# Optimization experiments

Hardware: AMD Instinct MI355X
Metric: run time of the kernel (lower is better)

## Reference

```python
import jax, jax.numpy as jnp
import numpy as np

D = 1024
N_HEAD = 16
D_HEAD = D // N_HEAD
EPS = 1e-6


def setup_inputs() -> dict:
    key = jax.random.key(0)
    k1, k2, k3 = jax.random.split(key, 3)
    x = jax.random.normal(k1, (4, 1024, D), dtype=jnp.float32)
    # Linear weights stored as (in, out); y = x @ W
    Wqkv = jax.random.normal(k2, (D, 3 * D), dtype=jnp.float32) * (1.0 / np.sqrt(D))
    Wo = jax.random.normal(k3, (D, D), dtype=jnp.float32) * (1.0 / np.sqrt(D))
    scale_q = jnp.ones((D_HEAD,), dtype=jnp.float32)
    scale_k = jnp.ones((D_HEAD,), dtype=jnp.float32)
    return {"x": x, "Wqkv": Wqkv, "Wo": Wo, "scale_q": scale_q, "scale_k": scale_k}


def _rmsnorm_global(x, scale):
    # NOTE: faithful to source: mean over ALL elements (scalar RMS), not per-vector.
    rms = jnp.sqrt(jnp.mean(x * x))
    return (x / (rms + EPS)) * scale  # scale broadcasts over last dim (d_head)


def reference(x, Wqkv, Wo, scale_q, scale_k):
    b, s, d = x.shape
    qkv = x @ Wqkv  # (b, s, 3d)
    q, k, v = jnp.split(qkv, 3, axis=-1)
    q = q.reshape(b, s, N_HEAD, D_HEAD)
    k = k.reshape(b, s, N_HEAD, D_HEAD)
    v = v.reshape(b, s, N_HEAD, D_HEAD)
    q = _rmsnorm_global(q, scale_q)
    k = _rmsnorm_global(k, scale_k)
    # NOTE: no 1/sqrt(d_head) scaling, no mask (faithful to source)
    attn = jnp.einsum('bqhd,bkhd->bhqk', q, k)
    attn = jax.nn.softmax(attn, axis=-1)
    z = jnp.einsum('bhqk,bkhd->bqhd', attn, v)
    z = z.reshape(b, s, d)
    return z @ Wo
```

## Files before the change

### kernel.cpp

```cpp
#include <hip/hip_runtime.h>

typedef float f32x4 __attribute__((ext_vector_type(4)));
typedef short bf16x8 __attribute__((ext_vector_type(8)));
typedef _Float16 f16x8 __attribute__((ext_vector_type(8)));
typedef unsigned short u16;

__device__ __forceinline__ u16 f2bf(float f) {
  unsigned int u = __float_as_uint(f);
  u = u + 0x7fffu + ((u >> 16) & 1u);
  return (u16)(u >> 16);
}
__device__ __forceinline__ float bf2f(u16 h) {
  return __uint_as_float(((unsigned int)h) << 16);
}
__device__ __forceinline__ u16 f2h(float f) {
  _Float16 h = (_Float16)f;
  union { _Float16 h; u16 u; } cv;
  cv.h = h;
  return cv.u;
}

typedef unsigned int as1_uint __attribute__((address_space(1)));
typedef unsigned int as3_uint __attribute__((address_space(3)));
__device__ __forceinline__ void gl_lds16(const void* g, void* l) {
  __builtin_amdgcn_global_load_lds((as1_uint*)g, (as3_uint*)l, 16, 0, 0);
}


__global__ __launch_bounds__(256) void conv_x_kernel(const float* __restrict__ x,
                                                     u16* __restrict__ Xp) {
  const int g = blockIdx.x * 256 + threadIdx.x;
  const int o = g * 8;
  const int slab = o >> 17;
  const int rem = o & 131071;
  const int kstep = rem >> 12;
  const int rem2 = rem & 4095;
  const int r = rem2 >> 5;
  const int cp = (rem2 & 31) >> 3;
  const int c = cp ^ ((r >> 1) & 3);
  const int s = slab * 128 + r;
  const int k = kstep * 32 + c * 8;
  const float4 v0 = *(const float4*)&x[(size_t)s * 1024 + k];
  const float4 v1 = *(const float4*)&x[(size_t)s * 1024 + k + 4];
  ushort4 a, b;
  a.x = f2h(v0.x); a.y = f2h(v0.y); a.z = f2h(v0.z); a.w = f2h(v0.w);
  b.x = f2h(v1.x); b.y = f2h(v1.y); b.z = f2h(v1.z); b.w = f2h(v1.w);
  *(ushort4*)&Xp[o] = a;
  *(ushort4*)&Xp[o + 4] = b;
}

__global__ __launch_bounds__(256) void conv_w_kernel(
    const float* __restrict__ src, int ncols, u16* __restrict__ dst) {
  __shared__ float tl[64][132];
  const int t = threadIdx.x;
  const int slab = blockIdx.x, kg = blockIdx.y;
  const int n0 = slab * 128, k0 = kg * 64;
#pragma unroll
  for (int i = 0; i < 8; i++) {
    const int fidx = i * 256 + t;
    const int r = fidx >> 5, c4 = (fidx & 31) * 4;
    *(float4*)&tl[r][c4] = *(const float4*)&src[(size_t)(k0 + r) * ncols + n0 + c4];
  }
  __syncthreads();
  const size_t base = (size_t)slab * 131072 + (size_t)(kg * 2) * 4096;
#pragma unroll
  for (int i = 0; i < 4; i++) {
    const int g = i * 256 + t;
    const int img = g >> 9, ci = g & 511;
    const int r = ci >> 2, cp = ci & 3;
    const int c = cp ^ ((r >> 1) & 3);
    const int klc = img * 32 + c * 8;
    ushort4 h0, h1;
    float v[8];
#pragma unroll
    for (int e = 0; e < 8; e++) v[e] = tl[klc + e][r];
    h0.x = f2h(v[0]); h0.y = f2h(v[1]); h0.z = f2h(v[2]); h0.w = f2h(v[3]);
    h1.x = f2h(v[4]); h1.y = f2h(v[5]); h1.z = f2h(v[6]); h1.w = f2h(v[7]);
    *(ushort4*)&dst[base + g * 8] = h0;
    *(ushort4*)&dst[base + g * 8 + 4] = h1;
  }
}

__global__ __launch_bounds__(512, 2) void gemm_qkv_kernel(
    const u16* __restrict__ Xp, const u16* __restrict__ Wp,
    u16* __restrict__ qf, u16* __restrict__ kf, u16* __restrict__ vT,
    const float* __restrict__ scale_q, const float* __restrict__ scale_k,
    float* __restrict__ sums) {
  __shared__ u16 SA[2][4][4096];
  __shared__ u16 SB[2][4][4096];
  const int tid = threadIdx.x, wv = tid >> 6, lane = tid & 63;
  const int lm = lane & 15, quad = lane >> 4;
  const int wvM = wv >> 2, wvN = wv & 3;
  const int L = blockIdx.x;
  const int xcd = L & 7, idx = L >> 3;
  const int bmT = (xcd & 3) * 4 + (idx & 3);
  const int bnT = (xcd >> 2) * 6 + (idx >> 2);
  const bool is_v = (bnT >= 8);
  const int fq = (quad ^ ((lm >> 1) & 3)) * 8;
  const int aOff = lm * 32 + fq;
  const u16* Xg = Xp + (size_t)bmT * 262144;
  const u16* Wg = Wp + (size_t)bnT * 262144;
  int bSub[4];
#pragma unroll
  for (int n = 0; n < 4; n++) {
    const int wn = wvN * 64 + n * 16;
    bSub[n] = ((wn >> 7) * 4096) + (wn & 127) * 32;
  }
  const u16* Ard = is_v ? &SA[0][0][0] : &SB[0][0][0];
  const u16* Brd = is_v ? &SB[0][0][0] : &SA[0][0][0];

  const f32x4 z4 = {0.f, 0.f, 0.f, 0.f};
  f32x4 acc[8][4];
#pragma unroll
  for (int i = 0; i < 8; i++)
#pragma unroll
    for (int j = 0; j < 4; j++) acc[i][j] = z4;

#define VMCNT4() asm volatile("s_waitcnt vmcnt(4)" ::: "memory")
#define VMCNT0() asm volatile("s_waitcnt vmcnt(0)" ::: "memory")
#define LGKM0() asm volatile("s_waitcnt lgkmcnt(0)" ::: "memory")
#define CFENCE() asm volatile("" ::: "memory")
#define SP1() __builtin_amdgcn_s_setprio(1)
#define SP0() __builtin_amdgcn_s_setprio(0)

#define QSTAGE(tt, nb, k2, sl)                                               \
  do {                                                                       \
    const size_t go_ = (size_t)(sl)*131072 + (size_t)(2 * (tt) + (k2)) * 4096\
                       + wv * 512 + lane * 8;                                \
    gl_lds16(Xg + go_, &SA[nb][(k2)*2 + (sl)][wv * 512]);                    \
    gl_lds16(Wg + go_, &SB[nb][(k2)*2 + (sl)][wv * 512]);                    \
  } while (0)

#define READ_A(BUF, k2, mq)                                                  \
  _Pragma("unroll")                                                          \
  for (int i = 0; i < 4; i++)                                                \
    afr[i] = *(const f16x8*)&Ard[(BUF)*16384 + ((k2)*2 + wvM) * 4096 +       \
                                 ((mq)*4 + i) * 512 + aOff];
#define READ_B(BUF, k2)                                                      \
  _Pragma("unroll")                                                          \
  for (int n = 0; n < 4; n++)                                                \
    bfr[n] = *(const f16x8*)&Brd[(BUF)*16384 + (k2)*8192 + bSub[n] + aOff];
#define MFMA16(mq)                                                           \
  _Pragma("unroll")                                                          \
  for (int i = 0; i < 4; i++)                                                \
    _Pragma("unroll")                                                        \
    for (int n = 0; n < 4; n++)                                              \
      acc[(mq)*4 + i][n] = __builtin_amdgcn_mfma_f32_16x16x32_f16(           \
          afr[i], bfr[n], acc[(mq)*4 + i][n], 0, 0, 0);

#define PH_WAIT_MFMA(mq)                                                     \
  CFENCE();                                                                  \
  __builtin_amdgcn_s_barrier();                                              \
  CFENCE();                                                                  \
  LGKM0();                                                                   \
  __builtin_amdgcn_sched_barrier(0);                                         \
  SP1();                                                                     \
  MFMA16(mq);                                                                \
  SP0()

#define KTILE(BUF, NBUF, t, DOSTAGE, GATE1, GATE3)                           \
  do {                                                                       \
    f16x8 bfr[4];                                                            \
    {                                                  \
      f16x8 afr[4];                                                          \
      READ_A(BUF, 0, 0);                                                     \
      READ_B(BUF, 0);                                                        \
      if (DOSTAGE) QSTAGE((t) + 1, NBUF, 0, 0);                              \
      PH_WAIT_MFMA(0);                                                       \
    }                                                                        \
    {                                                 \
      f16x8 afr[4];                                                          \
      READ_A(BUF, 0, 1);                                                     \
      if (DOSTAGE) QSTAGE((t) + 1, NBUF, 0, 1);                              \
      GATE1;        \
      PH_WAIT_MFMA(1);                                                       \
    }                                                                        \
    {                                                  \
      f16x8 afr[4];                                                          \
      READ_A(BUF, 1, 0);                                                     \
      READ_B(BUF, 1);                                                        \
      if (DOSTAGE) QSTAGE((t) + 1, NBUF, 1, 0);                              \
      PH_WAIT_MFMA(0);                                                       \
    }                                                                        \
    {                                                 \
      f16x8 afr[4];                                                          \
      READ_A(BUF, 1, 1);                                                     \
      if (DOSTAGE) QSTAGE((t) + 1, NBUF, 1, 1);                              \
      GATE3;   \
      PH_WAIT_MFMA(1);                                                       \
    }                                                                        \
    \
    \
    CFENCE();                                                                \
    __builtin_amdgcn_s_barrier();                                            \
    CFENCE();                                                                \
  } while (0)

  QSTAGE(0, 0, 0, 0);
  QSTAGE(0, 0, 0, 1);
  QSTAGE(0, 0, 1, 0);
  QSTAGE(0, 0, 1, 1);
  VMCNT4();
  __builtin_amdgcn_s_barrier();
  CFENCE();
#pragma unroll 1
  for (int t = 0; t < 14; t += 2) {
    KTILE(0, 1, t, true, VMCNT4(), VMCNT4());
    KTILE(1, 0, t + 1, true, VMCNT4(), VMCNT4());
  }
  KTILE(0, 1, 14, true, VMCNT4(), VMCNT4());
  KTILE(1, 0, 15, false, VMCNT0(), (void)0);
#undef KTILE
#undef PH_WAIT_MFMA
#undef READ_A
#undef READ_B
#undef MFMA16
#undef QSTAGE

  const int bn = bnT * 256, bm = bmT * 256;
  if (!is_v) {
    const bool is_k = (bnT >= 4);
    u16* dst = is_k ? kf : qf;
    float ss = 0.f;
#pragma unroll
    for (int mi = 0; mi < 8; mi++) {
      const int col0 = bn + wvM * 128 + mi * 16 + quad * 4;
      const int hh = (col0 >> 6) & 15, d0 = col0 & 63;
      const int dhi = d0 >> 5, cc = (d0 & 31) >> 3, eo = d0 & 7;
      float sc[4] = {1.f, 1.f, 1.f, 1.f};
      if (is_k) {
        const float4 sq = *(const float4*)&scale_q[d0];
        const float4 sk = *(const float4*)&scale_k[d0];
        sc[0] = sq.x * sk.x; sc[1] = sq.y * sk.y;
        sc[2] = sq.z * sk.z; sc[3] = sq.w * sk.w;
      }
#pragma unroll
      for (int ni = 0; ni < 4; ni++) {
        const int s = bm + wvN * 64 + ni * 16 + lm;
        const int b = s >> 10, sl = s & 1023, st = sl >> 6, r = sl & 63;
        const size_t off = ((size_t)((b * 16 + hh) * 16 + st)) * 4096 +
                           dhi * 2048 + r * 32 + ((cc ^ ((r >> 1) & 3)) * 8) + eo;
        ushort4 h4;
#pragma unroll
        for (int i = 0; i < 4; i++) {
          const float a = acc[mi][ni][i];
          ss += a * a;
          const u16 hv = f2h(a * sc[i]);
          if (i == 0) h4.x = hv;
          else if (i == 1) h4.y = hv;
          else if (i == 2) h4.z = hv;
          else h4.w = hv;
        }
        *(ushort4*)&dst[off] = h4;
      }
    }
#pragma unroll
    for (int m = 32; m >= 1; m >>= 1) ss += __shfl_xor(ss, m, 64);
    if (lane == 0) atomicAdd(&sums[is_k ? 1 : 0], ss);
  } else {
#pragma unroll
    for (int ni = 0; ni < 4; ni++) {
      const int col = (bn - 2048) + wvN * 64 + ni * 16 + lm;
      const int d = col & 63, hh = col >> 6;
#pragma unroll
      for (int mi = 0; mi < 8; mi++) {
        const int s0 = bm + wvM * 128 + mi * 16 + quad * 4;
        const int b = s0 >> 10, sl = s0 & 1023, st = sl >> 6;
        const int sh = (sl & 63) >> 5, cc = (sl & 31) >> 3, eo = sl & 7;
        const size_t off = ((size_t)((b * 16 + hh) * 16 + st)) * 4096 +
                           sh * 2048 + d * 32 + ((cc ^ ((d >> 1) & 3)) * 8) + eo;
        ushort4 v4;
        v4.x = f2bf(acc[mi][ni][0]);
        v4.y = f2bf(acc[mi][ni][1]);
        v4.z = f2bf(acc[mi][ni][2]);
        v4.w = f2bf(acc[mi][ni][3]);
        *(ushort4*)&vT[off] = v4;
      }
    }
  }
#undef VMCNT4
#undef VMCNT0
#undef LGKM0
#undef CFENCE
#undef SP1
#undef SP0
}

__global__ __launch_bounds__(256) void attn_kernel(
    const u16* __restrict__ qf, const u16* __restrict__ kf,
    const u16* __restrict__ vT, const float* __restrict__ sums,
    u16* __restrict__ z) {
  __shared__ u16 Ks0[4096], Vs0[4096], Ks1[4096], Vs1[4096];
  __shared__ u16 pb[4][2][16][64];
  const int tid = threadIdx.x, wv = tid >> 6, lane = tid & 63;
  const int lm = lane & 15, quad = lane >> 4;
  const int fq = (quad ^ ((lm >> 1) & 3)) * 8;
  const int L = blockIdx.x;
  const int xcd = L & 7, idx = L >> 3;
  const int qt8 = idx & 7, p = idx >> 3;
  const int pair = xcd * 8 + p;
  const int hh = pair & 15, b = pair >> 4;
  const float inv_rq = 1.f / (sqrtf(sums[0] * (1.f / 4194304.f)) + 1e-6f);
  const float inv_rk = 1.f / (sqrtf(sums[1] * (1.f / 4194304.f)) + 1e-6f);
  const float cs = inv_rq * inv_rk;
  const size_t hb = ((size_t)(b * 16 + hh)) * 65536;
  const u16* Kg = kf + hb;
  const u16* Vg = vT + hb;
  const int dof = wv * 1024;

  f16x8 aF[2][2];
#pragma unroll
  for (int qs = 0; qs < 2; qs++) {
    const int soff = wv * 32 + qs * 16;
    const size_t qb = hb + (size_t)(qt8 * 2 + (soff >> 6)) * 4096 +
                      (size_t)((soff & 63) + lm) * 32 + fq;
    aF[qs][0] = *(const f16x8*)&qf[qb];
    aF[qs][1] = *(const f16x8*)&qf[qb + 2048];
  }
  const f32x4 zz = {0.f, 0.f, 0.f, 0.f};
  f32x4 zac[2][4];
#pragma unroll
  for (int qs = 0; qs < 2; qs++)
#pragma unroll
    for (int dt = 0; dt < 4; dt++) zac[qs][dt] = zz;
  float rs[2] = {0.f, 0.f};

#define AISSUE(it, Ks, Vs)                                    \
  do {                                                        \
    const size_t tb_ = (size_t)(it) * 4096;                   \
    gl_lds16(Kg + tb_ + dof + lane * 8, &Ks[dof]);            \
    gl_lds16(Kg + tb_ + dof + 512 + lane * 8, &Ks[dof + 512]);\
    gl_lds16(Vg + tb_ + dof + lane * 8, &Vs[dof]);            \
    gl_lds16(Vg + tb_ + dof + 512 + lane * 8, &Vs[dof + 512]);\
  } while (0)

#define ATTN_BODY(it, Ks, Vs, Kn, Vn, do_issue)                               \
  do {                                                                        \
                                         \
    f16x8 kf0[4], kf1[4];                                                     \
    bf16x8 bv[2][4];                                                          \
_Pragma("unroll")                                                             \
    for (int nt = 0; nt < 4; nt++) {                                          \
      const int ro = (nt * 16 + lm) * 32 + fq;                                \
      kf0[nt] = *(const f16x8*)&Ks[ro];                                       \
      kf1[nt] = *(const f16x8*)&Ks[2048 + ro];                                \
    }                                                                         \
_Pragma("unroll")                                                             \
    for (int ch = 0; ch < 2; ch++)                                            \
_Pragma("unroll")                                                             \
      for (int dt = 0; dt < 4; dt++)                                          \
        bv[ch][dt] = *(const bf16x8*)&Vs[ch * 2048 + (dt * 16 + lm) * 32 + fq];\
    if (do_issue) AISSUE((it) + 1, Kn, Vn);                                   \
               \
_Pragma("unroll")                                                             \
    for (int qs = 0; qs < 2; qs++) {                                          \
_Pragma("unroll")                                                             \
      for (int nt = 0; nt < 4; nt++) {                                        \
        f32x4 c = zz;                                                         \
        c = __builtin_amdgcn_mfma_f32_16x16x32_f16(kf0[nt], aF[qs][0], c, 0, 0, 0);\
        c = __builtin_amdgcn_mfma_f32_16x16x32_f16(kf1[nt], aF[qs][1], c, 0, 0, 0);\
        const int k4 = nt * 4 + quad;                                         \
        const int sw = (k4 & 8) | ((k4 ^ lm) & 7);                            \
        ushort4 pw;                                                           \
        float p0 = __expf(c[0] * cs - 60.f);                                  \
        float p1 = __expf(c[1] * cs - 60.f);                                  \
        float p2 = __expf(c[2] * cs - 60.f);                                  \
        float p3 = __expf(c[3] * cs - 60.f);                                  \
        rs[qs] += (p0 + p1) + (p2 + p3);                                      \
        pw.x = f2bf(p0); pw.y = f2bf(p1); pw.z = f2bf(p2); pw.w = f2bf(p3);   \
        *(ushort4*)&pb[wv][qs][lm][sw * 4] = pw;                              \
      }                                                                       \
    }                                                                         \
           \
_Pragma("unroll")                                                             \
    for (int ch = 0; ch < 2; ch++) {                                          \
_Pragma("unroll")                                                             \
      for (int qs = 0; qs < 2; qs++) {                                        \
        const int k4a = ch * 8 + quad * 2, k4b = k4a + 1;                     \
        const ushort4 lo4 =                                                   \
            *(const ushort4*)&pb[wv][qs][lm][((k4a & 8) | ((k4a ^ lm) & 7)) * 4];\
        const ushort4 hi4 =                                                   \
            *(const ushort4*)&pb[wv][qs][lm][((k4b & 8) | ((k4b ^ lm) & 7)) * 4];\
        bf16x8 ap;                                                            \
        ap[0] = (short)lo4.x; ap[1] = (short)lo4.y;                           \
        ap[2] = (short)lo4.z; ap[3] = (short)lo4.w;                           \
        ap[4] = (short)hi4.x; ap[5] = (short)hi4.y;                           \
        ap[6] = (short)hi4.z; ap[7] = (short)hi4.w;                           \
_Pragma("unroll")                                                             \
        for (int dt = 0; dt < 4; dt++)                                        \
          zac[qs][dt] = __builtin_amdgcn_mfma_f32_16x16x32_bf16(              \
              bv[ch][dt], ap, zac[qs][dt], 0, 0, 0);                          \
      }                                                                       \
    }                                                                         \
  } while (0)

  AISSUE(0, Ks0, Vs0);
  for (int it = 0; it < 16; it += 2) {
    __syncthreads();
    ATTN_BODY(it, Ks0, Vs0, Ks1, Vs1, true);
    __syncthreads();
    ATTN_BODY(it + 1, Ks1, Vs1, Ks0, Vs0, (it + 2 < 16));
  }
#undef AISSUE
#undef ATTN_BODY

#pragma unroll
  for (int qs = 0; qs < 2; qs++) {
    rs[qs] += __shfl_xor(rs[qs], 16, 64);
    rs[qs] += __shfl_xor(rs[qs], 32, 64);
  }
  const int slab = b * 8 + qt8;
#pragma unroll
  for (int qs = 0; qs < 2; qs++) {
    const float inv = 1.f / rs[qs];
    const int r = wv * 32 + qs * 16 + lm;
#pragma unroll
    for (int dt = 0; dt < 4; dt++) {
      const int kstep = hh * 2 + (dt >> 1);
      const int d0 = dt * 16 + quad * 4;
      const int cc = (d0 & 31) >> 3, eo = d0 & 7;
      const size_t off = ((size_t)(slab * 32 + kstep)) * 4096 + r * 32 +
                         ((cc ^ ((r >> 1) & 3)) * 8) + eo;
      ushort4 o;
      o.x = f2h(zac[qs][dt][0] * inv);
      o.y = f2h(zac[qs][dt][1] * inv);
      o.z = f2h(zac[qs][dt][2] * inv);
      o.w = f2h(zac[qs][dt][3] * inv);
      *(ushort4*)&z[off] = o;
    }
  }
}

__global__ __launch_bounds__(256) void gemm_o_kernel(const u16* __restrict__ Wop,
                                                     const u16* __restrict__ zp,
                                                     float* __restrict__ out) {
  __shared__ u16 As0[4096], Bs0[4096], As1[4096], Bs1[4096];
  const int tid = threadIdx.x, wv = tid >> 6, lane = tid & 63;
  const int lm = lane & 15, quad = lane >> 4;
  const int wr = (wv >> 1) * 64, wc = (wv & 1) * 64;
  const int fq = (quad ^ ((lm >> 1) & 3)) * 8;
  const int L = blockIdx.x;
  const int xcd = L & 7, idx = L >> 3;
  const int rr = idx & 7, cc8 = idx >> 3;
  const int zpS = (xcd & 3) * 8 + rr;
  const int woS = (xcd >> 2) * 4 + cc8;
  const u16* Ag = Wop + (size_t)woS * 131072;
  const u16* Bg = zp + (size_t)zpS * 131072;
  const int dof0 = (wv * 2) * 512, dof1 = (wv * 2 + 1) * 512;
  const f32x4 z4 = {0.f, 0.f, 0.f, 0.f};
  f32x4 acc[4][4];
#pragma unroll
  for (int i = 0; i < 4; i++)
#pragma unroll
    for (int j = 0; j < 4; j++) acc[i][j] = z4;

#define ISSUE(t, As, Bs)                                   \
  do {                                                     \
    const size_t tb_ = (size_t)(t) * 4096;                 \
    gl_lds16(Ag + tb_ + dof0 + lane * 8, &As[dof0]);       \
    gl_lds16(Ag + tb_ + dof1 + lane * 8, &As[dof1]);       \
    gl_lds16(Bg + tb_ + dof0 + lane * 8, &Bs[dof0]);       \
    gl_lds16(Bg + tb_ + dof1 + lane * 8, &Bs[dof1]);       \
  } while (0)
#define GBODY(As, Bs)                                                     \
  do {                                                                    \
    f16x8 afr[4], bfr[4];                                                 \
_Pragma("unroll")                                                         \
    for (int mi = 0; mi < 4; mi++)                                        \
      afr[mi] = *(const f16x8*)&As[(wr + mi * 16 + lm) * 32 + fq];        \
_Pragma("unroll")                                                         \
    for (int ni = 0; ni < 4; ni++)                                        \
      bfr[ni] = *(const f16x8*)&Bs[(wc + ni * 16 + lm) * 32 + fq];        \
    DO_ISSUE;                                                             \
_Pragma("unroll")                                                         \
    for (int mi = 0; mi < 4; mi++)                                        \
_Pragma("unroll")                                                         \
      for (int ni = 0; ni < 4; ni++)                                      \
        acc[mi][ni] = __builtin_amdgcn_mfma_f32_16x16x32_f16(             \
            afr[mi], bfr[ni], acc[mi][ni], 0, 0, 0);                      \
  } while (0)

  ISSUE(0, As0, Bs0);
  for (int t = 0; t < 32; t += 2) {
    __syncthreads();
#define DO_ISSUE ISSUE(t + 1, As1, Bs1)
    GBODY(As0, Bs0);
#undef DO_ISSUE
    __syncthreads();
#define DO_ISSUE if (t + 2 < 32) ISSUE(t + 2, As0, Bs0)
    GBODY(As1, Bs1);
#undef DO_ISSUE
  }
#undef ISSUE
#undef GBODY

#pragma unroll
  for (int mi = 0; mi < 4; mi++) {
    const int col0 = woS * 128 + wr + mi * 16 + quad * 4;
#pragma unroll
    for (int ni = 0; ni < 4; ni++) {
      const int s = zpS * 128 + wc + ni * 16 + lm;
      const float4 o = {acc[mi][ni][0], acc[mi][ni][1], acc[mi][ni][2],
                        acc[mi][ni][3]};
      *(float4*)&out[(size_t)s * 1024 + col0] = o;
    }
  }
}

extern "C" void kernel_launch(void* const* d_in, const int* in_sizes, int n_in,
                              void* d_out, int out_size, void* d_ws,
                              size_t ws_size, hipStream_t stream) {
  (void)in_sizes; (void)n_in; (void)out_size; (void)ws_size;
  const float* x = (const float*)d_in[0];
  const float* Wqkv = (const float*)d_in[1];
  const float* Wo = (const float*)d_in[2];
  const float* scale_q = (const float*)d_in[3];
  const float* scale_k = (const float*)d_in[4];
  float* out = (float*)d_out;

  char* ws = (char*)d_ws;
  u16* qf = (u16*)(ws + 0);
  u16* kf = (u16*)(ws + 8388608);
  u16* Xp = (u16*)(ws + 16777216);
  u16* vT = (u16*)(ws + 25165824);
  u16* Wp = (u16*)(ws + 33554432);
  u16* zp = Xp;
  u16* Wop = Wp;
  float* sums = (float*)(ws + 39845888);

  conv_x_kernel<<<2048, 256, 0, stream>>>(x, Xp);
  conv_w_kernel<<<dim3(24, 16), 256, 0, stream>>>(Wqkv, 3072, Wp);
  hipMemsetAsync(sums, 0, 2 * sizeof(float), stream);
  gemm_qkv_kernel<<<192, 512, 0, stream>>>(Xp, Wp, qf, kf, vT,
                                           scale_q, scale_k, sums);
  conv_w_kernel<<<dim3(8, 16), 256, 0, stream>>>(Wo, 1024, Wop);
  attn_kernel<<<512, 256, 0, stream>>>(qf, kf, vT, sums, zp);
  gemm_o_kernel<<<256, 256, 0, stream>>>(Wop, zp, out);
}
```

Measured before the change: 183.4 us.

## Load attention K/V fragments directly from global memory instead of LDS staging

The attention kernel stops staging K and V tiles through double-buffered shared memory via async global-to-LDS copies and block barriers. Each wave now reads its K and V MFMA fragments straight from global memory (relying on L2/cache since all four waves read the same tiles), and the P scratch buffer is double-buffered by iteration parity instead. This removes the __syncthreads barriers and most LDS traffic and frees LDS for occupancy, at the cost of redundant global/L2 reads by each wave and no explicit prefetch of the next tile.

```diff
diff --git a/kernel.cpp b/kernel.cpp
--- a/kernel.cpp
+++ b/kernel.cpp
@@ -290,8 +290,7 @@
     const u16* __restrict__ qf, const u16* __restrict__ kf,
     const u16* __restrict__ vT, const float* __restrict__ sums,
     u16* __restrict__ z) {
-  __shared__ u16 Ks0[4096], Vs0[4096], Ks1[4096], Vs1[4096];
-  __shared__ u16 pb[4][2][16][64];
+  __shared__ u16 pb[2][4][2][16][64];
   const int tid = threadIdx.x, wv = tid >> 6, lane = tid & 63;
   const int lm = lane & 15, quad = lane >> 4;
   const int fq = (quad ^ ((lm >> 1) & 3)) * 8;
@@ -306,7 +305,6 @@
   const size_t hb = ((size_t)(b * 16 + hh)) * 65536;
   const u16* Kg = kf + hb;
   const u16* Vg = vT + hb;
-  const int dof = wv * 1024;
 
   f16x8 aF[2][2];
 #pragma unroll
@@ -325,84 +323,64 @@
     for (int dt = 0; dt < 4; dt++) zac[qs][dt] = zz;
   float rs[2] = {0.f, 0.f};
 
-#define AISSUE(it, Ks, Vs)                                    \
-  do {                                                        \
-    const size_t tb_ = (size_t)(it) * 4096;                   \
-    gl_lds16(Kg + tb_ + dof + lane * 8, &Ks[dof]);            \
-    gl_lds16(Kg + tb_ + dof + 512 + lane * 8, &Ks[dof + 512]);\
-    gl_lds16(Vg + tb_ + dof + lane * 8, &Vs[dof]);            \
-    gl_lds16(Vg + tb_ + dof + 512 + lane * 8, &Vs[dof + 512]);\
-  } while (0)
-
-#define ATTN_BODY(it, Ks, Vs, Kn, Vn, do_issue)                               \
-  do {                                                                        \
-                                         \
-    f16x8 kf0[4], kf1[4];                                                     \
-    bf16x8 bv[2][4];                                                          \
-_Pragma("unroll")                                                             \
-    for (int nt = 0; nt < 4; nt++) {                                          \
-      const int ro = (nt * 16 + lm) * 32 + fq;                                \
-      kf0[nt] = *(const f16x8*)&Ks[ro];                                       \
-      kf1[nt] = *(const f16x8*)&Ks[2048 + ro];                                \
-    }                                                                         \
-_Pragma("unroll")                                                             \
-    for (int ch = 0; ch < 2; ch++)                                            \
-_Pragma("unroll")                                                             \
-      for (int dt = 0; dt < 4; dt++)                                          \
-        bv[ch][dt] = *(const bf16x8*)&Vs[ch * 2048 + (dt * 16 + lm) * 32 + fq];\
-    if (do_issue) AISSUE((it) + 1, Kn, Vn);                                   \
-               \
-_Pragma("unroll")                                                             \
-    for (int qs = 0; qs < 2; qs++) {                                          \
-_Pragma("unroll")                                                             \
-      for (int nt = 0; nt < 4; nt++) {                                        \
-        f32x4 c = zz;                                                         \
-        c = __builtin_amdgcn_mfma_f32_16x16x32_f16(kf0[nt], aF[qs][0], c, 0, 0, 0);\
-        c = __builtin_amdgcn_mfma_f32_16x16x32_f16(kf1[nt], aF[qs][1], c, 0, 0, 0);\
-        const int k4 = nt * 4 + quad;                                         \
-        const int sw = (k4 & 8) | ((k4 ^ lm) & 7);                            \
-        ushort4 pw;                                                           \
-        float p0 = __expf(c[0] * cs - 60.f);                                  \
-        float p1 = __expf(c[1] * cs - 60.f);                                  \
-        float p2 = __expf(c[2] * cs - 60.f);                                  \
-        float p3 = __expf(c[3] * cs - 60.f);                                  \
-        rs[qs] += (p0 + p1) + (p2 + p3);                                      \
-        pw.x = f2bf(p0); pw.y = f2bf(p1); pw.z = f2bf(p2); pw.w = f2bf(p3);   \
-        *(ushort4*)&pb[wv][qs][lm][sw * 4] = pw;                              \
-      }                                                                       \
-    }                                                                         \
-           \
-_Pragma("unroll")                                                             \
-    for (int ch = 0; ch < 2; ch++) {                                          \
-_Pragma("unroll")                                                             \
-      for (int qs = 0; qs < 2; qs++) {                                        \
-        const int k4a = ch * 8 + quad * 2, k4b = k4a + 1;                     \
-        const ushort4 lo4 =                                                   \
-            *(const ushort4*)&pb[wv][qs][lm][((k4a & 8) | ((k4a ^ lm) & 7)) * 4];\
-        const ushort4 hi4 =                                                   \
-            *(const ushort4*)&pb[wv][qs][lm][((k4b & 8) | ((k4b ^ lm) & 7)) * 4];\
-        bf16x8 ap;                                                            \
-        ap[0] = (short)lo4.x; ap[1] = (short)lo4.y;                           \
-        ap[2] = (short)lo4.z; ap[3] = (short)lo4.w;                           \
-        ap[4] = (short)hi4.x; ap[5] = (short)hi4.y;                           \
-        ap[6] = (short)hi4.z; ap[7] = (short)hi4.w;                           \
-_Pragma("unroll")                                                             \
-        for (int dt = 0; dt < 4; dt++)                                        \
-          zac[qs][dt] = __builtin_amdgcn_mfma_f32_16x16x32_bf16(              \
-              bv[ch][dt], ap, zac[qs][dt], 0, 0, 0);                          \
-      }                                                                       \
-    }                                                                         \
-  } while (0)
-
-  AISSUE(0, Ks0, Vs0);
-  for (int it = 0; it < 16; it += 2) {
-    __syncthreads();
-    ATTN_BODY(it, Ks0, Vs0, Ks1, Vs1, true);
-    __syncthreads();
-    ATTN_BODY(it + 1, Ks1, Vs1, Ks0, Vs0, (it + 2 < 16));
-  }
-#undef AISSUE
-#undef ATTN_BODY
+#pragma unroll 2
+  for (int it = 0; it < 16; ++it) {
+    const int par = it & 1;
+    const u16* Kt = Kg + (size_t)it * 4096;
+    const u16* Vt = Vg + (size_t)it * 4096;
+    f16x8 kf0[4], kf1[4];
+    bf16x8 bv[2][4];
+#pragma unroll
+    for (int nt = 0; nt < 4; nt++) {
+      const int ro = (nt * 16 + lm) * 32 + fq;
+      kf0[nt] = *(const f16x8*)&Kt[ro];
+      kf1[nt] = *(const f16x8*)&Kt[2048 + ro];
+    }
+#pragma unroll
+    for (int ch = 0; ch < 2; ch++)
+#pragma unroll
+      for (int dt = 0; dt < 4; dt++)
+        bv[ch][dt] = *(const bf16x8*)&Vt[ch * 2048 + (dt * 16 + lm) * 32 + fq];
+#pragma unroll
+    for (int qs = 0; qs < 2; qs++) {
+#pragma unroll
+      for (int nt = 0; nt < 4; nt++) {
+        f32x4 c = zz;
+        c = __builtin_amdgcn_mfma_f32_16x16x32_f16(kf0[nt], aF[qs][0], c, 0, 0, 0);
+        c = __builtin_amdgcn_mfma_f32_16x16x32_f16(kf1[nt], aF[qs][1], c, 0, 0, 0);
+        const int k4 = nt * 4 + quad;
+        const int sw = (k4 & 8) | ((k4 ^ lm) & 7);
+        ushort4 pw;
+        float p0 = __expf(c[0] * cs - 60.f);
+        float p1 = __expf(c[1] * cs - 60.f);
+        float p2 = __expf(c[2] * cs - 60.f);
+        float p3 = __expf(c[3] * cs - 60.f);
+        rs[qs] += (p0 + p1) + (p2 + p3);
+        pw.x = f2bf(p0); pw.y = f2bf(p1); pw.z = f2bf(p2); pw.w = f2bf(p3);
+        *(ushort4*)&pb[par][wv][qs][lm][sw * 4] = pw;
+      }
+    }
+#pragma unroll
+    for (int ch = 0; ch < 2; ch++) {
+#pragma unroll
+      for (int qs = 0; qs < 2; qs++) {
+        const int k4a = ch * 8 + quad * 2, k4b = k4a + 1;
+        const ushort4 lo4 =
+            *(const ushort4*)&pb[par][wv][qs][lm][((k4a & 8) | ((k4a ^ lm) & 7)) * 4];
+        const ushort4 hi4 =
+            *(const ushort4*)&pb[par][wv][qs][lm][((k4b & 8) | ((k4b ^ lm) & 7)) * 4];
+        bf16x8 ap;
+        ap[0] = (short)lo4.x; ap[1] = (short)lo4.y;
+        ap[2] = (short)lo4.z; ap[3] = (short)lo4.w;
+        ap[4] = (short)hi4.x; ap[5] = (short)hi4.y;
+        ap[6] = (short)hi4.z; ap[7] = (short)hi4.w;
+#pragma unroll
+        for (int dt = 0; dt < 4; dt++)
+          zac[qs][dt] = __builtin_amdgcn_mfma_f32_16x16x32_bf16(
+              bv[ch][dt], ap, zac[qs][dt], 0, 0, 0);
+      }
+    }
+  }
 
 #pragma unroll
   for (int qs = 0; qs < 2; qs++) {
```

New measurement: 184.2 us. About the same (+0.4%).
